# Performance work log

Hardware: AMD Instinct MI355X
Metric: run time of the kernel (lower is better)

The kernel has to match this reference:

```python
import jax, jax.numpy as jnp
import numpy as np

B, H, V, L, T = 64, 512, 32000, 3, 38
SOS = 0  # word2idx['<SOS>']


def setup_inputs() -> dict:
    key = jax.random.key(0)
    ks = jax.random.split(key, 16)
    s = 0.05
    rn = lambda k, shape: jax.random.normal(k, shape, jnp.float32) * s
    return {
        "feat": jax.random.normal(ks[0], (B, H), jnp.float32),
        "W_ih0": rn(ks[1], (4 * H, 2 * H)),
        "W_hh0": rn(ks[2], (4 * H, H)),
        "W_ih_rest": rn(ks[3], (L - 1, 4 * H, H)),
        "W_hh_rest": rn(ks[4], (L - 1, 4 * H, H)),
        "b_ih": rn(ks[5], (L, 4 * H)),
        "b_hh": rn(ks[6], (L, 4 * H)),
        "embed": rn(ks[7], (V, H)),
        "W_proj": rn(ks[8], (V, H)),
        "b_proj": rn(ks[9], (V,)),
        "W_hid": rn(ks[10], (H, H)),
        "b_hid": rn(ks[11], (H,)),
        "W_enc": rn(ks[12], (H, H)),
        "b_enc": rn(ks[13], (H,)),
        "W_attout": rn(ks[14], (1, H)),
        "b_attout": rn(ks[15], (1,)),
    }


def _lstm_cell(x, h, c, Wih, Whh, bih, bhh):
    # PyTorch gate order: i, f, g, o
    g = x @ Wih.T + h @ Whh.T + bih + bhh
    i, f, gg, o = jnp.split(g, 4, axis=-1)
    c2 = jax.nn.sigmoid(f) * c + jax.nn.sigmoid(i) * jnp.tanh(gg)
    h2 = jax.nn.sigmoid(o) * jnp.tanh(c2)
    return h2, c2


def _forward(feat, W_ih0, W_hh0, W_ih_rest, W_hh_rest, b_ih, b_hh,
             embed, W_proj, b_proj, W_hid, b_hid, W_enc, b_enc,
             W_attout, b_attout):
    # encoder 'sequence': pooled feature repeated over L decoder layers -> [L,B,H]
    enc = jnp.broadcast_to(feat[None], (L, B, H))
    enc_p = enc @ W_enc.T + b_enc  # precompute encoder projection (constant over steps)

    def attn(hbar):  # hbar = sum(hidden_layers)/L, [B,H]  (Bahdanau additive attention)
        e = (jnp.tanh(enc_p + (hbar @ W_hid.T + b_hid)[None]) @ W_attout.T + b_attout)[..., 0]  # [L,B]
        w = jax.nn.softmax(e, axis=0)  # softmax over encoder positions
        return jnp.einsum('lb,lbh->bh', w, enc)  # context [B,H]

    def lstm(inp, h, c):  # one time-step through the 3-layer stacked LSTM
        h0, c0 = _lstm_cell(inp, h[0], c[0], W_ih0, W_hh0, b_ih[0], b_hh[0])
        h1, c1 = _lstm_cell(h0, h[1], c[1], W_ih_rest[0], W_hh_rest[0], b_ih[1], b_hh[1])
        h2, c2 = _lstm_cell(h1, h[2], c[2], W_ih_rest[1], W_hh_rest[1], b_ih[2], b_hh[2])
        return jnp.stack([h0, h1, h2]), jnp.stack([c0, c1, c2])

    ctx0 = attn(feat)  # initial hidden = feat repeated L times -> mean = feat
    start = jnp.broadcast_to(embed[SOS], (B, H))
    h = jnp.broadcast_to(ctx0[None], (L, B, H))
    c = h
    inp0 = jnp.concatenate([ctx0, start], axis=-1)  # [B, 2H]

    def step(carry, _):
        h, c, inp = carry
        h, c = lstm(inp, h, c)
        out = h[-1]  # [B,H]
        ids = jnp.argmax(out @ W_proj.T + b_proj, axis=-1)  # greedy token (dropout in eval mode)
        emb = embed[ids]  # [B,H]
        ctx = attn(emb / L)  # addMask averages with 1/decoder_layer weights
        return (h, c, jnp.concatenate([ctx, emb], axis=-1)), out

    _, outs = jax.lax.scan(step, (h, c, inp0), None, length=T - 1)  # outs [T-1,B,H]
    pred = jnp.concatenate([start[None], outs], axis=0)  # [T,B,H]
    # final projection, permuted to [B, V, T] as in the torch module
    return jnp.einsum('tbh,vh->bvt', pred, W_proj) + b_proj[None, :, None]


def reference(feat, W_ih0, W_hh0, W_ih_rest, W_hh_rest, b_ih, b_hh,
              embed, W_proj, b_proj, W_hid, b_hid, W_enc, b_enc,
              W_attout, b_attout):
    return _forward(feat, W_ih0, W_hh0, W_ih_rest, W_hh_rest, b_ih, b_hh,
                    embed, W_proj, b_proj, W_hid, b_hid, W_enc, b_enc,
                    W_attout, b_attout)
```

## Files before the change

kernel.cpp:

```cpp
#include <hip/hip_runtime.h>
#include <hip/hip_bf16.h>

#define B   64
#define H   512
#define V   32000
#define T   38
#define G4  2048
#define NSTEP 37
#define VT  64
#define KC  64
#define LDP 68

__device__ __forceinline__ float sigf(float x){ return 1.0f/(1.0f + expf(-x)); }

__device__ __forceinline__ unsigned int fkey(float x){
  unsigned int u = __float_as_uint(x);
  return (u & 0x80000000u) ? ~u : (u | 0x80000000u);
}

__global__ __launch_bounds__(256) void k_init_state(const float* __restrict__ feat,
                                                    float* __restrict__ hT, float* __restrict__ cT,
                                                    unsigned long long* __restrict__ packed){
  int idx = blockIdx.x*blockDim.x + threadIdx.x;
  if (idx < 3*H*B){
    int b = idx & (B-1);
    int k = (idx >> 6) & (H-1);
    float v = feat[(size_t)b*H + k];
    hT[idx] = v;
    cT[idx] = v;
  }
  if (idx < NSTEP*B) packed[idx] = 0ULL;
}

__global__ __launch_bounds__(256) void k_gfeat(const float* __restrict__ feat,
                                               const float* __restrict__ Wih0,
                                               const float* __restrict__ b_ih,
                                               const float* __restrict__ b_hh,
                                               float* __restrict__ gfeatT){
  int j = blockIdx.x;
  int b = threadIdx.x;
  int gate = threadIdx.y;
  int r = gate*H + j;
  const float* w = Wih0 + (size_t)r*(2*H);
  const float* x = feat + (size_t)b*H;
  float acc = 0.f;
  #pragma unroll 4
  for (int k=0;k<H;k++) acc = fmaf(w[k], x[k], acc);
  gfeatT[((size_t)gate*H + j)*B + b] = acc + b_ih[r] + b_hh[r];
}

__global__ __launch_bounds__(256) void k_row0(const float* __restrict__ embed_,
                                              const float* __restrict__ Wp,
                                              const float* __restrict__ bp,
                                              float* __restrict__ dst, int mode){
  int v = blockIdx.x*blockDim.x + threadIdx.x;
  if (v >= V) return;
  const float4* e = (const float4*)embed_;
  const float4* w = (const float4*)(Wp + (size_t)v*H);
  float acc = 0.f;
  #pragma unroll 4
  for (int k=0;k<H/4;k++){
    float4 a = e[k], c = w[k];
    acc += a.x*c.x + a.y*c.y + a.z*c.z + a.w*c.w;
  }
  acc += bp[v];
  if (mode == 0){
    for (int b=0;b<B;b++) dst[(size_t)b*V + v] = acc;
  } else {
    for (int b=0;b<B;b++) dst[((size_t)b*V + v)*T] = acc;
  }
}

__global__ __launch_bounds__(256) void k_lstm(int layer, int s,
    const float* __restrict__ Wih, const float* __restrict__ Whh,
    const float* __restrict__ bias_ih, const float* __restrict__ bias_hh,
    const float* __restrict__ gfeatT,
    const float* __restrict__ embed_,
    const unsigned long long* __restrict__ packedPrev,
    const float* __restrict__ xLowerT,
    const float* __restrict__ hOldT,
    float* __restrict__ hNewT,
    float* __restrict__ cT_)
{
  const int j  = blockIdx.x;
  const int b  = threadIdx.x;
  const int ks = threadIdx.y;
  __shared__ float part[4][4][B];

  const int kbase = (ks & 1)*256;
  const float *w0,*w1,*w2,*w3;
  const float* xptr = nullptr;
  const float* eptr = nullptr;

  if (ks < 2){
    if (layer == 0){
      const size_t gs = (size_t)H*(2*H);
      w0 = Wih + (size_t)j*(2*H) + H + kbase;
      w1 = w0 + gs; w2 = w0 + 2*gs; w3 = w0 + 3*gs;
      int er = 0;
      if (s > 0) er = (int)(~(unsigned int)(packedPrev[b] & 0xFFFFFFFFull));
      eptr = embed_ + (size_t)er*H + kbase;
    } else {
      const size_t gs = (size_t)H*H;
      w0 = Wih + (size_t)j*H + kbase;
      w1 = w0 + gs; w2 = w0 + 2*gs; w3 = w0 + 3*gs;
      xptr = xLowerT + (size_t)kbase*B + b;
    }
  } else {
    const size_t gs = (size_t)H*H;
    w0 = Whh + (size_t)j*H + kbase;
    w1 = w0 + gs; w2 = w0 + 2*gs; w3 = w0 + 3*gs;
    xptr = hOldT + (size_t)kbase*B + b;
  }

  float a0=0.f, a1=0.f, a2=0.f, a3=0.f;
  if (eptr){
    #pragma unroll 4
    for (int k=0;k<256;k++){
      float xv = eptr[k];
      a0 = fmaf(w0[k], xv, a0); a1 = fmaf(w1[k], xv, a1);
      a2 = fmaf(w2[k], xv, a2); a3 = fmaf(w3[k], xv, a3);
    }
  } else {
    #pragma unroll 4
    for (int k=0;k<256;k++){
      float xv = xptr[(size_t)k*B];
      a0 = fmaf(w0[k], xv, a0); a1 = fmaf(w1[k], xv, a1);
      a2 = fmaf(w2[k], xv, a2); a3 = fmaf(w3[k], xv, a3);
    }
  }
  part[ks][0][b]=a0; part[ks][1][b]=a1; part[ks][2][b]=a2; part[ks][3][b]=a3;
  __syncthreads();

  if (ks == 0){
    float g[4];
    #pragma unroll
    for (int gt=0; gt<4; gt++){
      float sum = part[0][gt][b] + part[1][gt][b] + part[2][gt][b] + part[3][gt][b];
      if (layer == 0) sum += gfeatT[((size_t)gt*H + j)*B + b];
      else            sum += bias_ih[gt*H + j] + bias_hh[gt*H + j];
      g[gt] = sum;
    }
    float i_ = sigf(g[0]);
    float f_ = sigf(g[1]);
    float gg = tanhf(g[2]);
    float o_ = sigf(g[3]);
    float cold = cT_[(size_t)j*B + b];
    float c2 = f_*cold + i_*gg;
    float h2 = o_*tanhf(c2);
    cT_[(size_t)j*B + b]  = c2;
    hNewT[(size_t)j*B + b] = h2;
  }
}

__global__ __launch_bounds__(256) void k_logits(
    const float* __restrict__ h2T,
    const float* __restrict__ Wp,
    const float* __restrict__ bp,
    float* __restrict__ dst, int strideV, int strideB,
    unsigned long long* __restrict__ packedS)
{
  __shared__ float Wt[KC][LDP];
  __shared__ float Xt[KC][LDP];
  __shared__ unsigned long long red[B][17];

  const int tid = threadIdx.x;
  const int v0  = blockIdx.x * VT;
  const int tv  = tid & 15;
  const int tb  = tid >> 4;
  const int vr  = tid >> 2;
  const int kq  = tid & 3;

  float acc[4][4];
  #pragma unroll
  for (int i=0;i<4;i++)
    #pragma unroll
    for (int q=0;q<4;q++) acc[i][q] = 0.f;

  for (int k0=0; k0<H; k0+=KC){
    __syncthreads();
    const float* wsrc = Wp + (size_t)(v0+vr)*H + k0 + kq*16;
    #pragma unroll
    for (int i=0;i<4;i++){
      float4 w4 = *(const float4*)(wsrc + i*4);
      int kk = kq*16 + i*4;
      Wt[kk+0][vr]=w4.x; Wt[kk+1][vr]=w4.y; Wt[kk+2][vr]=w4.z; Wt[kk+3][vr]=w4.w;
    }
    const float* xsrc = h2T + (size_t)(k0+vr)*B + kq*16;
    #pragma unroll
    for (int i=0;i<4;i++){
      float4 x4 = *(const float4*)(xsrc + i*4);
      int bb = kq*16 + i*4;
      Xt[vr][bb+0]=x4.x; Xt[vr][bb+1]=x4.y; Xt[vr][bb+2]=x4.z; Xt[vr][bb+3]=x4.w;
    }
    __syncthreads();
    #pragma unroll 8
    for (int k=0;k<KC;k++){
      float4 w4 = *(const float4*)&Wt[k][tv<<2];
      float4 x4 = *(const float4*)&Xt[k][tb<<2];
      acc[0][0]=fmaf(x4.x,w4.x,acc[0][0]); acc[0][1]=fmaf(x4.x,w4.y,acc[0][1]);
      acc[0][2]=fmaf(x4.x,w4.z,acc[0][2]); acc[0][3]=fmaf(x4.x,w4.w,acc[0][3]);
      acc[1][0]=fmaf(x4.y,w4.x,acc[1][0]); acc[1][1]=fmaf(x4.y,w4.y,acc[1][1]);
      acc[1][2]=fmaf(x4.y,w4.z,acc[1][2]); acc[1][3]=fmaf(x4.y,w4.w,acc[1][3]);
      acc[2][0]=fmaf(x4.z,w4.x,acc[2][0]); acc[2][1]=fmaf(x4.z,w4.y,acc[2][1]);
      acc[2][2]=fmaf(x4.z,w4.z,acc[2][2]); acc[2][3]=fmaf(x4.z,w4.w,acc[2][3]);
      acc[3][0]=fmaf(x4.w,w4.x,acc[3][0]); acc[3][1]=fmaf(x4.w,w4.y,acc[3][1]);
      acc[3][2]=fmaf(x4.w,w4.z,acc[3][2]); acc[3][3]=fmaf(x4.w,w4.w,acc[3][3]);
    }
  }

  float4 bb4 = *(const float4*)(bp + v0 + (tv<<2));
  float barr[4] = {bb4.x, bb4.y, bb4.z, bb4.w};
  float vals[4][4];
  #pragma unroll
  for (int bj=0;bj<4;bj++)
    #pragma unroll
    for (int vi=0;vi<4;vi++) vals[bj][vi] = acc[bj][vi] + barr[vi];

  if (strideV == 1){
    #pragma unroll
    for (int bj=0;bj<4;bj++){
      int b = (tb<<2)+bj;
      *(float4*)(dst + (size_t)b*strideB + v0 + (tv<<2)) =
          make_float4(vals[bj][0], vals[bj][1], vals[bj][2], vals[bj][3]);
    }
  } else {
    #pragma unroll
    for (int bj=0;bj<4;bj++){
      int b = (tb<<2)+bj;
      #pragma unroll
      for (int vi=0;vi<4;vi++)
        dst[(size_t)b*strideB + (size_t)(v0+(tv<<2)+vi)*strideV] = vals[bj][vi];
    }
  }

  #pragma unroll
  for (int bj=0;bj<4;bj++){
    float m = vals[bj][0]; int mi = v0+(tv<<2);
    #pragma unroll
    for (int vi=1;vi<4;vi++){
      if (vals[bj][vi] > m){ m = vals[bj][vi]; mi = v0+(tv<<2)+vi; }
    }
    unsigned long long key = ((unsigned long long)fkey(m)<<32)
                           | (unsigned long long)(unsigned int)(~(unsigned int)mi);
    red[(tb<<2)+bj][tv] = key;
  }
  __syncthreads();
  if (tid < B){
    unsigned long long best = red[tid][0];
    #pragma unroll
    for (int t2=1;t2<16;t2++){ unsigned long long k2 = red[tid][t2]; if (k2 > best) best = k2; }
    atomicMax(packedS + tid, best);
  }
}

__global__ __launch_bounds__(256) void k_transpose(const float* __restrict__ stage,
                                                   float* __restrict__ out){
  int idx = blockIdx.x*blockDim.x + threadIdx.x;
  float vals[T];
  #pragma unroll
  for (int t=0;t<T;t++) vals[t] = stage[(size_t)t*B*V + idx];
  float2* o = (float2*)(out + (size_t)idx*T);
  #pragma unroll
  for (int t=0;t<T;t+=2) o[t>>1] = make_float2(vals[t], vals[t+1]);
}

extern "C" void kernel_launch(void* const* d_in, const int* in_sizes, int n_in,
                              void* d_out, int out_size, void* d_ws, size_t ws_size,
                              hipStream_t stream){
  const float* feat      = (const float*)d_in[0];
  const float* W_ih0     = (const float*)d_in[1];
  const float* W_hh0     = (const float*)d_in[2];
  const float* W_ih_rest = (const float*)d_in[3];
  const float* W_hh_rest = (const float*)d_in[4];
  const float* b_ih      = (const float*)d_in[5];
  const float* b_hh      = (const float*)d_in[6];
  const float* embed     = (const float*)d_in[7];
  const float* W_proj    = (const float*)d_in[8];
  const float* b_proj    = (const float*)d_in[9];
  float* out = (float*)d_out;

  char* ws = (char*)d_ws;
  size_t off = 0;
  float* hT = (float*)(ws + off); off += (size_t)2*3*H*B*4;
  float* cT = (float*)(ws + off); off += (size_t)3*H*B*4;
  float* gfeatT = (float*)(ws + off); off += (size_t)4*H*B*4;
  unsigned long long* packed = (unsigned long long*)(ws + off); off += (size_t)NSTEP*B*8;
  off = (off + 255) & ~(size_t)255;
  float* stage = (float*)(ws + off);
  const size_t stageBytes = (size_t)T*B*V*4;
  const bool staged = (ws_size >= off + stageBytes);

  dim3 bl64x4(64,4);
  k_init_state<<<(3*H*B + 255)/256, 256, 0, stream>>>(feat, hT, cT, packed);
  k_gfeat<<<H, bl64x4, 0, stream>>>(feat, W_ih0, b_ih, b_hh, gfeatT);
  if (staged) k_row0<<<(V+255)/256, 256, 0, stream>>>(embed, W_proj, b_proj, stage, 0);
  else        k_row0<<<(V+255)/256, 256, 0, stream>>>(embed, W_proj, b_proj, out, 1);

  const size_t LHB = (size_t)H*B;
  for (int s=0; s<NSTEP; s++){
    const int p = s & 1, q = p ^ 1;
    float* hOld = hT + (size_t)p*3*LHB;
    float* hNew = hT + (size_t)q*3*LHB;
    const unsigned long long* pk = packed + (size_t)(s>0 ? s-1 : 0)*B;

    k_lstm<<<H, bl64x4, 0, stream>>>(0, s, W_ih0, W_hh0,
        b_ih, b_hh, gfeatT, embed, pk,
        (const float*)nullptr, hOld + 0*LHB, hNew + 0*LHB, cT + 0*LHB);
    k_lstm<<<H, bl64x4, 0, stream>>>(1, s, W_ih_rest, W_hh_rest,
        b_ih + 1*G4, b_hh + 1*G4, (const float*)nullptr, (const float*)nullptr,
        (const unsigned long long*)nullptr,
        hNew + 0*LHB, hOld + 1*LHB, hNew + 1*LHB, cT + 1*LHB);
    k_lstm<<<H, bl64x4, 0, stream>>>(2, s, W_ih_rest + (size_t)G4*H, W_hh_rest + (size_t)G4*H,
        b_ih + 2*G4, b_hh + 2*G4, (const float*)nullptr, (const float*)nullptr,
        (const unsigned long long*)nullptr,
        hNew + 1*LHB, hOld + 2*LHB, hNew + 2*LHB, cT + 2*LHB);

    if (staged)
      k_logits<<<V/VT, 256, 0, stream>>>(hNew + 2*LHB, W_proj, b_proj,
          stage + (size_t)(s+1)*B*V, 1, V, packed + (size_t)s*B);
    else
      k_logits<<<V/VT, 256, 0, stream>>>(hNew + 2*LHB, W_proj, b_proj,
          out + (s+1), T, V*T, packed + (size_t)s*B);
  }

  if (staged) k_transpose<<<(B*V)/256, 256, 0, stream>>>(stage, out);
}
```

Measured before the change: 4.715 ms.

## Compute per-step vocab logits with bf16 MFMA and rescue argmax exactly

Converts W_proj to bf16 once and computes each step's 64x32000 logits with bf16 MFMA instructions instead of the fp32 tiled kernel. An approximate argmax is taken from these logits, then a rescue kernel recomputes in fp32 every candidate within a fixed margin of the approximate max, so the greedy token choice stays exact. The logits written to the output are now bf16-precision, which adds error to the stored values, and the rescue pass adds a full-row scan per batch row each step.

```diff
diff --git a/kernel.cpp b/kernel.cpp
--- a/kernel.cpp
+++ b/kernel.cpp
@@ -10,6 +10,10 @@
 #define VT  64
 #define KC  64
 #define LDP 68
+#define DELTA 0.125f
+
+typedef __attribute__((ext_vector_type(8))) short short8;
+typedef __attribute__((ext_vector_type(4))) float f32x4;
 
 __device__ __forceinline__ float sigf(float x){ return 1.0f/(1.0f + expf(-x)); }
 
@@ -17,10 +21,20 @@
   unsigned int u = __float_as_uint(x);
   return (u & 0x80000000u) ? ~u : (u | 0x80000000u);
 }
+__device__ __forceinline__ float fromkey(unsigned int k){
+  unsigned int u = (k & 0x80000000u) ? (k & 0x7fffffffu) : ~k;
+  return __uint_as_float(u);
+}
+__device__ __forceinline__ unsigned short f2bf(float x){
+  unsigned int u = __float_as_uint(x);
+  unsigned int r = (u + 0x7FFFu + ((u >> 16) & 1u)) >> 16;
+  return (unsigned short)r;
+}
 
 __global__ __launch_bounds__(256) void k_init_state(const float* __restrict__ feat,
                                                     float* __restrict__ hT, float* __restrict__ cT,
-                                                    unsigned long long* __restrict__ packed){
+                                                    unsigned long long* __restrict__ packed,
+                                                    unsigned long long* __restrict__ apprx){
   int idx = blockIdx.x*blockDim.x + threadIdx.x;
   if (idx < 3*H*B){
     int b = idx & (B-1);
@@ -29,7 +43,15 @@
     hT[idx] = v;
     cT[idx] = v;
   }
-  if (idx < NSTEP*B) packed[idx] = 0ULL;
+  if (idx < NSTEP*B){ packed[idx] = 0ULL; apprx[idx] = 0ULL; }
+}
+
+__global__ __launch_bounds__(256) void k_convW(const float* __restrict__ src,
+                                               unsigned short* __restrict__ dstW){
+  int i = blockIdx.x*blockDim.x + threadIdx.x;
+  float4 f = ((const float4*)src)[i];
+  ushort4 u = make_ushort4(f2bf(f.x), f2bf(f.y), f2bf(f.z), f2bf(f.w));
+  ((ushort4*)dstW)[i] = u;
 }
 
 __global__ __launch_bounds__(256) void k_gfeat(const float* __restrict__ feat,
@@ -64,11 +86,8 @@
     acc += a.x*c.x + a.y*c.y + a.z*c.z + a.w*c.w;
   }
   acc += bp[v];
-  if (mode == 0){
-    for (int b=0;b<B;b++) dst[(size_t)b*V + v] = acc;
-  } else {
-    for (int b=0;b<B;b++) dst[((size_t)b*V + v)*T] = acc;
-  }
+  if (mode == 0){ for (int b=0;b<B;b++) dst[(size_t)b*V + v] = acc; }
+  else          { for (int b=0;b<B;b++) dst[((size_t)b*V + v)*T] = acc; }
 }
 
 __global__ __launch_bounds__(256) void k_lstm(int layer, int s,
@@ -80,7 +99,8 @@
     const float* __restrict__ xLowerT,
     const float* __restrict__ hOldT,
     float* __restrict__ hNewT,
-    float* __restrict__ cT_)
+    float* __restrict__ cT_,
+    unsigned short* __restrict__ hBf)
 {
   const int j  = blockIdx.x;
   const int b  = threadIdx.x;
@@ -150,7 +170,148 @@
     float h2 = o_*tanhf(c2);
     cT_[(size_t)j*B + b]  = c2;
     hNewT[(size_t)j*B + b] = h2;
-  }
+    if (hBf) hBf[(size_t)b*H + j] = f2bf(h2);
+  }
+}
+
+__global__ __launch_bounds__(256) void k_logits_mfma(
+    const unsigned short* __restrict__ Wbf,
+    const unsigned short* __restrict__ h2bf,
+    const float* __restrict__ bp,
+    float* __restrict__ dst, int strideV, int strideB,
+    unsigned long long* __restrict__ apprxS)
+{
+  const int tid  = threadIdx.x;
+  const int wave = tid >> 6;
+  const int lane = tid & 63;
+  const int col  = lane & 15;
+  const int grp  = lane >> 4;
+  const int v0   = blockIdx.x*128 + wave*32;
+
+  f32x4 acc[4][2] = {{{0.f,0.f,0.f,0.f},{0.f,0.f,0.f,0.f}},
+                     {{0.f,0.f,0.f,0.f},{0.f,0.f,0.f,0.f}},
+                     {{0.f,0.f,0.f,0.f},{0.f,0.f,0.f,0.f}},
+                     {{0.f,0.f,0.f,0.f},{0.f,0.f,0.f,0.f}}};
+
+  const unsigned short* hp = h2bf + (size_t)col*H + grp*8;
+  const unsigned short* wp = Wbf  + (size_t)(v0+col)*H + grp*8;
+
+  for (int k0 = 0; k0 < H; k0 += 32){
+    short8 afr[4], bfr[2];
+    #pragma unroll
+    for (int bt=0;bt<4;bt++)
+      afr[bt] = *(const short8*)(hp + (size_t)bt*16*H + k0);
+    #pragma unroll
+    for (int vt=0;vt<2;vt++)
+      bfr[vt] = *(const short8*)(wp + (size_t)vt*16*H + k0);
+    #pragma unroll
+    for (int bt=0;bt<4;bt++)
+      #pragma unroll
+      for (int vt=0;vt<2;vt++)
+        acc[bt][vt] = __builtin_amdgcn_mfma_f32_16x16x32_bf16(afr[bt], bfr[vt], acc[bt][vt], 0,0,0);
+  }
+
+  float bias0 = bp[v0 + col];
+  float bias1 = bp[v0 + 16 + col];
+
+  unsigned long long keys[4][4];
+  #pragma unroll
+  for (int bt=0;bt<4;bt++){
+    #pragma unroll
+    for (int r=0;r<4;r++){
+      int b = bt*16 + grp*4 + r;
+      float val0 = acc[bt][0][r] + bias0;
+      float val1 = acc[bt][1][r] + bias1;
+      if (strideV == 1){
+        dst[(size_t)b*strideB + v0 + col]      = val0;
+        dst[(size_t)b*strideB + v0 + 16 + col] = val1;
+      } else {
+        dst[(size_t)b*strideB + (size_t)(v0+col)*strideV]    = val0;
+        dst[(size_t)b*strideB + (size_t)(v0+16+col)*strideV] = val1;
+      }
+      float m; int mv;
+      if (val1 > val0){ m = val1; mv = v0+16+col; } else { m = val0; mv = v0+col; }
+      keys[bt][r] = ((unsigned long long)fkey(m)<<32)
+                  | (unsigned long long)(unsigned int)(~(unsigned int)mv);
+    }
+  }
+  #pragma unroll
+  for (int bt=0;bt<4;bt++)
+    #pragma unroll
+    for (int r=0;r<4;r++){
+      unsigned long long k2 = keys[bt][r];
+      #pragma unroll
+      for (int m=1;m<16;m<<=1){
+        unsigned long long o = __shfl_xor(k2, m, 64);
+        if (o > k2) k2 = o;
+      }
+      keys[bt][r] = k2;
+    }
+
+  __shared__ unsigned long long wred[4][64];
+  if (col == 0){
+    #pragma unroll
+    for (int bt=0;bt<4;bt++)
+      #pragma unroll
+      for (int r=0;r<4;r++)
+        wred[wave][bt*16 + grp*4 + r] = keys[bt][r];
+  }
+  __syncthreads();
+  if (tid < 64){
+    unsigned long long best = wred[0][tid];
+    #pragma unroll
+    for (int w=1;w<4;w++) if (wred[w][tid] > best) best = wred[w][tid];
+    atomicMax(apprxS + tid, best);
+  }
+}
+
+__global__ __launch_bounds__(256) void k_rescue(
+    const float* __restrict__ plane, int strideV, int strideB,
+    const float* __restrict__ hT2,
+    const float* __restrict__ Wp,
+    const float* __restrict__ bp,
+    const unsigned long long* __restrict__ apprxS,
+    unsigned long long* __restrict__ packedS)
+{
+  const int b   = blockIdx.x;
+  const int tid = threadIdx.x;
+  const float amax = fromkey((unsigned int)(apprxS[b] >> 32));
+  const float thresh = amax - DELTA;
+  const float* row = plane + (size_t)b*strideB;
+
+  unsigned long long best = 0ULL;
+  if (strideV == 1){
+    for (int v4 = 4*tid; v4 < V; v4 += 1024){
+      float4 f = *(const float4*)(row + v4);
+      float vv[4] = {f.x, f.y, f.z, f.w};
+      #pragma unroll
+      for (int i=0;i<4;i++){
+        if (vv[i] >= thresh){
+          int v = v4 + i;
+          const float* wrow = Wp + (size_t)v*H;
+          float acc = 0.f;
+          for (int k=0;k<H;k++) acc = fmaf(wrow[k], hT2[(size_t)k*B + b], acc);
+          float exact = acc + bp[v];
+          unsigned long long key = ((unsigned long long)fkey(exact)<<32)
+                                 | (unsigned long long)(unsigned int)(~(unsigned int)v);
+          if (key > best) best = key;
+        }
+      }
+    }
+  } else {
+    for (int v = tid; v < V; v += 256){
+      if (row[(size_t)v*strideV] >= thresh){
+        const float* wrow = Wp + (size_t)v*H;
+        float acc = 0.f;
+        for (int k=0;k<H;k++) acc = fmaf(wrow[k], hT2[(size_t)k*B + b], acc);
+        float exact = acc + bp[v];
+        unsigned long long key = ((unsigned long long)fkey(exact)<<32)
+                               | (unsigned long long)(unsigned int)(~(unsigned int)v);
+        if (key > best) best = key;
+      }
+    }
+  }
+  if (best) atomicMax(packedS + b, best);
 }
 
 __global__ __launch_bounds__(256) void k_logits(
@@ -286,14 +447,24 @@
   float* cT = (float*)(ws + off); off += (size_t)3*H*B*4;
   float* gfeatT = (float*)(ws + off); off += (size_t)4*H*B*4;
   unsigned long long* packed = (unsigned long long*)(ws + off); off += (size_t)NSTEP*B*8;
+  unsigned long long* apprx  = (unsigned long long*)(ws + off); off += (size_t)NSTEP*B*8;
+  unsigned short* h2bf = (unsigned short*)(ws + off); off += (size_t)B*H*2;
   off = (off + 255) & ~(size_t)255;
-  float* stage = (float*)(ws + off);
+  const size_t offA = off;
+  unsigned short* Wbf = (unsigned short*)(ws + offA);
+  size_t offB = offA + (size_t)V*H*2;
+  offB = (offB + 255) & ~(size_t)255;
+
   const size_t stageBytes = (size_t)T*B*V*4;
-  const bool staged = (ws_size >= off + stageBytes);
+  const bool useMfma   = (ws_size >= offB);
+  const bool staged    = useMfma ? (ws_size >= offB + stageBytes)
+                                 : (ws_size >= offA + stageBytes);
+  float* stage = (float*)(ws + (useMfma ? offB : offA));
 
   dim3 bl64x4(64,4);
-  k_init_state<<<(3*H*B + 255)/256, 256, 0, stream>>>(feat, hT, cT, packed);
+  k_init_state<<<(3*H*B + 255)/256, 256, 0, stream>>>(feat, hT, cT, packed, apprx);
   k_gfeat<<<H, bl64x4, 0, stream>>>(feat, W_ih0, b_ih, b_hh, gfeatT);
+  if (useMfma) k_convW<<<(V*H/4)/256, 256, 0, stream>>>(W_proj, Wbf);
   if (staged) k_row0<<<(V+255)/256, 256, 0, stream>>>(embed, W_proj, b_proj, stage, 0);
   else        k_row0<<<(V+255)/256, 256, 0, stream>>>(embed, W_proj, b_proj, out, 1);
 
@@ -306,22 +477,31 @@
 
     k_lstm<<<H, bl64x4, 0, stream>>>(0, s, W_ih0, W_hh0,
         b_ih, b_hh, gfeatT, embed, pk,
-        (const float*)nullptr, hOld + 0*LHB, hNew + 0*LHB, cT + 0*LHB);
+        (const float*)nullptr, hOld + 0*LHB, hNew + 0*LHB, cT + 0*LHB,
+        (unsigned short*)nullptr);
     k_lstm<<<H, bl64x4, 0, stream>>>(1, s, W_ih_rest, W_hh_rest,
         b_ih + 1*G4, b_hh + 1*G4, (const float*)nullptr, (const float*)nullptr,
         (const unsigned long long*)nullptr,
-        hNew + 0*LHB, hOld + 1*LHB, hNew + 1*LHB, cT + 1*LHB);
+        hNew + 0*LHB, hOld + 1*LHB, hNew + 1*LHB, cT + 1*LHB,
+        (unsigned short*)nullptr);
     k_lstm<<<H, bl64x4, 0, stream>>>(2, s, W_ih_rest + (size_t)G4*H, W_hh_rest + (size_t)G4*H,
         b_ih + 2*G4, b_hh + 2*G4, (const float*)nullptr, (const float*)nullptr,
         (const unsigned long long*)nullptr,
-        hNew + 1*LHB, hOld + 2*LHB, hNew + 2*LHB, cT + 2*LHB);
-
-    if (staged)
+        hNew + 1*LHB, hOld + 2*LHB, hNew + 2*LHB, cT + 2*LHB,
+        useMfma ? h2bf : (unsigned short*)nullptr);
+
+    float* plane  = staged ? (stage + (size_t)(s+1)*B*V) : (out + (s+1));
+    int sv = staged ? 1 : T;
+    int sb = staged ? V : V*T;
+    if (useMfma){
+      k_logits_mfma<<<V/128, 256, 0, stream>>>(Wbf, h2bf, b_proj,
+          plane, sv, sb, apprx + (size_t)s*B);
+      k_rescue<<<B, 256, 0, stream>>>(plane, sv, sb,
+          hNew + 2*LHB, W_proj, b_proj, apprx + (size_t)s*B, packed + (size_t)s*B);
+    } else {
       k_logits<<<V/VT, 256, 0, stream>>>(hNew + 2*LHB, W_proj, b_proj,
-          stage + (size_t)(s+1)*B*V, 1, V, packed + (size_t)s*B);
-    else
-      k_logits<<<V/VT, 256, 0, stream>>>(hNew + 2*LHB, W_proj, b_proj,
-          out + (s+1), T, V*T, packed + (size_t)s*B);
+          plane, sv, sb, packed + (size_t)s*B);
+    }
   }
 
   if (staged) k_transpose<<<(B*V)/256, 256, 0, stream>>>(stage, out);
```

New measurement: 13.09 ms. 178% more time.
